# Optimization experiments

Hardware: AMD Instinct MI355X
Metric: run time of the kernel (lower is better)

The kernel has to match this reference:

```python
import jax, jax.numpy as jnp
import numpy as np

ROWS, N = 2048, 32768  # kernel requires N = 8 tiles * 1024 threads * 4 (float4)

def setup_inputs() -> dict:
    key = jax.random.key(0)
    kx, km = jax.random.split(key)
    x = jax.random.normal(kx, (ROWS, N), dtype=jnp.float32)
    mask = jax.random.randint(km, (ROWS, N), 0, 2).astype(jnp.bool_)
    return {"x": x, "mask": mask}

def reference(x, mask):
    # Masked inclusive cumulative sum along dim=1: cumsum(where(mask, x, 0))
    return jnp.cumsum(jnp.where(mask, x, jnp.float32(0)), axis=1)
```

## Files before the change

### kernel.cpp

```cpp
#include <hip/hip_runtime.h>


#define ROWS    2048
#define NCOL    32768
#define THREADS 1024
#define TILES   8

__global__ __launch_bounds__(THREADS, 2) void masked_cumsum_kernel(
    const float* __restrict__ x,
    const int*   __restrict__ mask,
    float*       __restrict__ out)
{
    const int row = blockIdx.x;
    const size_t base = (size_t)row * NCOL;
    const float4* __restrict__ xrow = (const float4*)(x + base);
    const int4*   __restrict__ mrow = (const int4*)(mask + base);
    float4*       __restrict__ orow = (float4*)(out + base);

    const int tid  = threadIdx.x;
    const int lane = tid & 63;
    const int wave = tid >> 6;

    __shared__ float wsum[16];

    float carry = 0.0f;

    float4 xv = xrow[tid];
    int4   mv = mrow[tid];

    #pragma unroll
    for (int t = 0; t < TILES; ++t) {
        float4 xn; int4 mn;
        if (t + 1 < TILES) {
            xn = xrow[(t + 1) * THREADS + tid];
            mn = mrow[(t + 1) * THREADS + tid];
        }

        float a0 = mv.x ? xv.x : 0.0f;
        float a1 = mv.y ? xv.y : 0.0f;
        float a2 = mv.z ? xv.z : 0.0f;
        float a3 = mv.w ? xv.w : 0.0f;
        float s0 = a0;
        float s1 = s0 + a1;
        float s2 = s1 + a2;
        float s3 = s2 + a3;

        float sc = s3;
        #pragma unroll
        for (int d = 1; d < 64; d <<= 1) {
            float o = __shfl_up(sc, d);
            if (lane >= d) sc += o;
        }

        if (lane == 63) wsum[wave] = sc;
        __syncthreads();

        float woff = 0.0f, total = 0.0f;
        #pragma unroll
        for (int w = 0; w < 16; ++w) {
            float ws = wsum[w];
            woff  += (w < wave) ? ws : 0.0f;
            total += ws;
        }

        float b = carry + woff + (sc - s3);
        orow[t * THREADS + tid] = make_float4(b + s0, b + s1, b + s2, b + s3);

        carry += total;
        xv = xn; mv = mn;
        __syncthreads();
    }
}

extern "C" void kernel_launch(void* const* d_in, const int* in_sizes, int n_in,
                              void* d_out, int out_size, void* d_ws, size_t ws_size,
                              hipStream_t stream) {
    const float* x    = (const float*)d_in[0];
    const int*   mask = (const int*)d_in[1];
    float*       out  = (float*)d_out;
    masked_cumsum_kernel<<<ROWS, THREADS, 0, stream>>>(x, mask, out);
}
```

Baseline: 584.2 us.

## Load whole row into registers and do a single block-wide scan via LDS

```diff
diff --git a/kernel.cpp b/kernel.cpp
--- a/kernel.cpp
+++ b/kernel.cpp
@@ -5,8 +5,9 @@
 #define NCOL    32768
 #define THREADS 1024
 #define TILES   8
+#define NCHUNK  (THREADS * TILES)
 
-__global__ __launch_bounds__(THREADS, 2) void masked_cumsum_kernel(
+__global__ __launch_bounds__(THREADS, 1) void masked_cumsum_kernel(
     const float* __restrict__ x,
     const int*   __restrict__ mask,
     float*       __restrict__ out)
@@ -21,54 +22,68 @@
     const int lane = tid & 63;
     const int wave = tid >> 6;
 
-    __shared__ float wsum[16];
+    __shared__ float csum[NCHUNK + NCHUNK / 8];
+    __shared__ float wtot[16];
 
-    float carry = 0.0f;
+    float4 xv[TILES];
+    int4   mv[TILES];
+    #pragma unroll
+    for (int t = 0; t < TILES; ++t) {
+        xv[t] = xrow[t * THREADS + tid];
+        mv[t] = mrow[t * THREADS + tid];
+    }
 
-    float4 xv = xrow[tid];
-    int4   mv = mrow[tid];
+    float4 p[TILES];
+    #pragma unroll
+    for (int t = 0; t < TILES; ++t) {
+        float a0 = mv[t].x ? xv[t].x : 0.0f;
+        float a1 = mv[t].y ? xv[t].y : 0.0f;
+        float a2 = mv[t].z ? xv[t].z : 0.0f;
+        float a3 = mv[t].w ? xv[t].w : 0.0f;
+        p[t].x = a0;
+        p[t].y = p[t].x + a1;
+        p[t].z = p[t].y + a2;
+        p[t].w = p[t].z + a3;
+        int c = t * THREADS + tid;
+        csum[c + (c >> 3)] = p[t].w;
+    }
+    __syncthreads();
+
+    float s[8];
+    float run = 0.0f;
+    #pragma unroll
+    for (int k = 0; k < 8; ++k) {
+        run += csum[tid * 9 + k];
+        s[k] = run;
+    }
+
+    float sc = run;
+    #pragma unroll
+    for (int d = 1; d < 64; d <<= 1) {
+        float o = __shfl_up(sc, d);
+        if (lane >= d) sc += o;
+    }
+    if (lane == 63) wtot[wave] = sc;
+    __syncthreads();
+
+    float woff = 0.0f;
+    #pragma unroll
+    for (int w = 0; w < 16; ++w)
+        woff += (w < wave) ? wtot[w] : 0.0f;
+
+    const float thr_excl = woff + (sc - run);
+
+    #pragma unroll
+    for (int k = 0; k < 8; ++k)
+        csum[tid * 9 + k] = thr_excl + (k ? s[k - 1] : 0.0f);
+    __syncthreads();
 
     #pragma unroll
     for (int t = 0; t < TILES; ++t) {
-        float4 xn; int4 mn;
-        if (t + 1 < TILES) {
-            xn = xrow[(t + 1) * THREADS + tid];
-            mn = mrow[(t + 1) * THREADS + tid];
-        }
-
-        float a0 = mv.x ? xv.x : 0.0f;
-        float a1 = mv.y ? xv.y : 0.0f;
-        float a2 = mv.z ? xv.z : 0.0f;
-        float a3 = mv.w ? xv.w : 0.0f;
-        float s0 = a0;
-        float s1 = s0 + a1;
-        float s2 = s1 + a2;
-        float s3 = s2 + a3;
-
-        float sc = s3;
-        #pragma unroll
-        for (int d = 1; d < 64; d <<= 1) {
-            float o = __shfl_up(sc, d);
-            if (lane >= d) sc += o;
-        }
-
-        if (lane == 63) wsum[wave] = sc;
-        __syncthreads();
-
-        float woff = 0.0f, total = 0.0f;
-        #pragma unroll
-        for (int w = 0; w < 16; ++w) {
-            float ws = wsum[w];
-            woff  += (w < wave) ? ws : 0.0f;
-            total += ws;
-        }
-
-        float b = carry + woff + (sc - s3);
-        orow[t * THREADS + tid] = make_float4(b + s0, b + s1, b + s2, b + s3);
-
-        carry += total;
-        xv = xn; mv = mn;
-        __syncthreads();
+        int c = t * THREADS + tid;
+        float off = csum[c + (c >> 3)];
+        orow[t * THREADS + tid] =
+            make_float4(off + p[t].x, off + p[t].y, off + p[t].z, off + p[t].w);
     }
 }
 
```

Result: faster. 570.2 us (-2.4%).
